# Kernel optimization log

Measured on AMD Instinct MI355X. Metric: run time of the kernel, lower is better.

The kernel has to match this reference:

```python
import jax, jax.numpy as jnp
import numpy as np

N_TOK = 4096      # total packed tokens
C = 256           # channels
H = 8             # num_heads
B = 8             # number of packed sequences
NEG = -10000.0    # additive mask value used by the torch module (not -inf)


def setup_inputs() -> dict:
    key = jax.random.key(0)
    ks = jax.random.split(key, 8)
    qkv = jax.random.normal(ks[0], (N_TOK, C), jnp.float32)
    q_pos = jax.random.normal(ks[1], (N_TOK, C), jnp.float32)
    # cu_seqlens: sorted prefix boundaries, 0 ... N_TOK (B segments)
    interior = jnp.sort(jax.random.randint(ks[2], (B - 1,), 1, N_TOK))
    cu_seqlens = jnp.concatenate([jnp.zeros((1,), jnp.int32),
                                  interior.astype(jnp.int32),
                                  jnp.full((1,), N_TOK, jnp.int32)])
    # xavier-uniform-ish scale for linear weights (stored as [in, out])
    def xavier(k, fan_in, fan_out):
        lim = np.sqrt(6.0 / (fan_in + fan_out)).astype(np.float32)
        return jax.random.uniform(k, (fan_in, fan_out), jnp.float32, -lim, lim)
    Wq = xavier(ks[3], C, C)
    Wkv = xavier(ks[4], C, 2 * C)
    Wproj = xavier(ks[5], C, C)
    bproj = jnp.zeros((C,), jnp.float32)
    return {"qkv": qkv, "q_pos": q_pos, "cu_seqlens": cu_seqlens,
            "max_seqlen": N_TOK, "Wq": Wq, "Wkv": Wkv,
            "Wproj": Wproj, "bproj": bproj}


def reference(qkv, q_pos, cu_seqlens, max_seqlen, Wq, Wkv, Wproj, bproj):
    N, Cdim = qkv.shape
    hd = Cdim // H
    scale = hd ** -0.5

    q = (qkv + q_pos) @ Wq                 # [N, C]
    kv = qkv @ Wkv                         # [N, 2C]
    k, v = kv[:, :Cdim], kv[:, Cdim:]

    # upcast_attention=True -> float32 attention (inputs already fp32)
    q = q.astype(jnp.float32).reshape(N, H, hd)
    k = k.astype(jnp.float32).reshape(N, H, hd)
    v = v.astype(jnp.float32).reshape(N, H, hd)

    # block-diagonal additive mask: segment id per token via searchsorted
    seg = jnp.searchsorted(cu_seqlens[1:], jnp.arange(N), side='right')
    bias = jnp.where(seg[:, None] == seg[None, :], 0.0, NEG)  # [N, N]

    scores = jnp.einsum('nhd,mhd->hnm', q, k) * scale + bias[None]  # [H,N,N]
    attn = jax.nn.softmax(scores, axis=-1)
    feat = jnp.einsum('hnm,mhd->nhd', attn, v).reshape(N, Cdim)
    feat = feat.astype(qkv.dtype)
    return feat @ Wproj + bproj
```

## Files before the change

### kernel.cpp

```cpp
#include <hip/hip_runtime.h>
#include <hip/hip_bf16.h>
#include <math.h>

#define NTOK 4096
#define CDIM 256
#define NH   8
#define HD   32
#define SCALE 0.17677669529663687f

typedef __attribute__((ext_vector_type(8))) short bf16x8;
typedef __attribute__((ext_vector_type(4))) short short4v;
typedef __attribute__((ext_vector_type(4))) float f32x4;

__device__ inline short f2b(float f) {
  union { __hip_bfloat16 h; short s; } u;
  u.h = __float2bfloat16(f);
  return u.s;
}
__device__ inline short4v pack4(f32x4 v) {
  short4v o; o[0] = f2b(v[0]); o[1] = f2b(v[1]); o[2] = f2b(v[2]); o[3] = f2b(v[3]);
  return o;
}

__global__ __launch_bounds__(256) void prep_kernel(
    const float* __restrict__ qkv, const float* __restrict__ qpos,
    const float* __restrict__ Wq, const float* __restrict__ Wkv,
    const float* __restrict__ Wp,
    short* __restrict__ Xq, short* __restrict__ X,
    short* __restrict__ WT, short* __restrict__ WpT)
{
  const int b = blockIdx.x, t = threadIdx.x;
  if (b < 1024) {
    const int i4 = (b * 256 + t) * 4;
    float4 a = *(const float4*)(qkv + i4);
    float4 p = *(const float4*)(qpos + i4);
    short4v xo, qo;
    xo[0] = f2b(a.x); xo[1] = f2b(a.y); xo[2] = f2b(a.z); xo[3] = f2b(a.w);
    qo[0] = f2b(a.x + p.x); qo[1] = f2b(a.y + p.y); qo[2] = f2b(a.z + p.z); qo[3] = f2b(a.w + p.w);
    *(short4v*)(X + i4)  = xo;
    *(short4v*)(Xq + i4) = qo;
  } else {
    const int gid = (b - 1024) * 256 + t;
    const int c  = gid & 1023;
    const int k4 = (gid >> 10) * 4;
    short4v o;
    if (c < 768) {
      #pragma unroll
      for (int j = 0; j < 4; ++j) {
        int k = k4 + j;
        float v = (c < 256) ? Wq[(size_t)k * 256 + c] * SCALE
                            : Wkv[(size_t)k * 512 + (c - 256)];
        o[j] = f2b(v);
      }
      *(short4v*)(WT + (size_t)c * 256 + k4) = o;
    } else {
      const int cc = c - 768;
      #pragma unroll
      for (int j = 0; j < 4; ++j) o[j] = f2b(Wp[(size_t)(k4 + j) * 256 + cc]);
      *(short4v*)(WpT + (size_t)cc * 256 + k4) = o;
    }
  }
}

__global__ __launch_bounds__(256) void gemm_qkv(
    const short* __restrict__ Xq, const short* __restrict__ X,
    const short* __restrict__ WT,
    short* __restrict__ qb, short* __restrict__ khp, short* __restrict__ vblk)
{
  __shared__ short Al[64][40];
  __shared__ short Wl[64][40];
  const int bx = blockIdx.x;
  const int n0 = blockIdx.y * 64;
  const int c0 = bx * 64;
  const int tid = threadIdx.x;
  const int w = tid >> 6, l = tid & 63, lg = l >> 4, lr = l & 15;
  const int wc = w & 1, wn = w >> 1;
  const short* A = (bx < 4) ? Xq : X;

  f32x4 acc[2][2];
  #pragma unroll
  for (int i = 0; i < 2; ++i)
    #pragma unroll
    for (int j = 0; j < 2; ++j) acc[i][j] = (f32x4){0.f, 0.f, 0.f, 0.f};

  for (int kt = 0; kt < 256; kt += 32) {
    __syncthreads();
    {
      int row = tid >> 2, seg = tid & 3;
      *(bf16x8*)&Al[row][seg * 8] = *(const bf16x8*)(A  + (size_t)(n0 + row) * 256 + kt + seg * 8);
      *(bf16x8*)&Wl[row][seg * 8] = *(const bf16x8*)(WT + (size_t)(c0 + row) * 256 + kt + seg * 8);
    }
    __syncthreads();
    bf16x8 wf[2], xf[2];
    #pragma unroll
    for (int ci = 0; ci < 2; ++ci) wf[ci] = *(bf16x8*)&Wl[wc * 32 + ci * 16 + lr][lg * 8];
    #pragma unroll
    for (int ni = 0; ni < 2; ++ni) xf[ni] = *(bf16x8*)&Al[wn * 32 + ni * 16 + lr][lg * 8];
    if (bx < 8) {
      #pragma unroll
      for (int ci = 0; ci < 2; ++ci)
        #pragma unroll
        for (int ni = 0; ni < 2; ++ni)
          acc[ci][ni] = __builtin_amdgcn_mfma_f32_16x16x32_bf16(wf[ci], xf[ni], acc[ci][ni], 0, 0, 0);
    } else {
      #pragma unroll
      for (int ci = 0; ci < 2; ++ci)
        #pragma unroll
        for (int ni = 0; ni < 2; ++ni)
          acc[ci][ni] = __builtin_amdgcn_mfma_f32_16x16x32_bf16(xf[ni], wf[ci], acc[ci][ni], 0, 0, 0);
    }
  }

  if (bx < 4) {
    const int cl0 = bx * 64;
    #pragma unroll
    for (int ci = 0; ci < 2; ++ci)
      #pragma unroll
      for (int ni = 0; ni < 2; ++ni) {
        int c = cl0 + wc * 32 + ci * 16 + lg * 4;
        int n = n0 + wn * 32 + ni * 16 + lr;
        *(short4v*)(qb + (size_t)n * 256 + c) = pack4(acc[ci][ni]);
      }
  } else if (bx < 8) {
    const int cl0 = (bx - 4) * 64;
    #pragma unroll
    for (int ci = 0; ci < 2; ++ci)
      #pragma unroll
      for (int ni = 0; ni < 2; ++ni) {
        int c = cl0 + wc * 32 + ci * 16 + lg * 4;
        int n = n0 + wn * 32 + ni * 16 + lr;
        int hh = c >> 5, d = c & 31;
        int tt = n >> 5, k = n & 31;
        int s = ((k >> 2) & 1) * 16 + (k >> 3) * 4 + (k & 3);
        *(short4v*)(khp + (((size_t)hh * 128 + tt) * 32 + s) * 32 + d) = pack4(acc[ci][ni]);
      }
  } else {
    const int cv0 = (bx - 8) * 64;
    #pragma unroll
    for (int ci = 0; ci < 2; ++ci)
      #pragma unroll
      for (int ni = 0; ni < 2; ++ni) {
        int c = cv0 + wc * 32 + ci * 16 + lr;
        int n = n0 + wn * 32 + ni * 16 + lg * 4;
        int hh = c >> 5, d = c & 31;
        int tt = n >> 5, k = n & 31;
        *(short4v*)(vblk + (((size_t)hh * 128 + tt) * 32 + d) * 32 + k) = pack4(acc[ci][ni]);
      }
  }
}

__global__ __launch_bounds__(256) void attn7(
    const short* __restrict__ qb, const short* __restrict__ khp,
    const short* __restrict__ vblk, const int* __restrict__ cu,
    short* __restrict__ featb)
{
  __shared__ float red[4][64][18];
  const int tid = threadIdx.x;
  const int w = tid >> 6, l = tid & 63, lg = l >> 4, lr = l & 15;
  const int bid = blockIdx.x;
  const int lid = ((bid & 7) << 7) | (bid >> 3);
  const int h = lid & 7, t32 = lid >> 3;
  const int n0 = t32 * 32;

  int cs[9];
  #pragma unroll
  for (int i = 0; i < 9; ++i) cs[i] = cu[i];

  const int qn0 = n0 + lr, qn1 = n0 + 16 + lr;
  int g0 = 0, g1 = 0, sg0 = 0, sgL = 0;
  #pragma unroll
  for (int j = 1; j <= 8; ++j) {
    g0  += (cs[j] <= qn0);
    g1  += (cs[j] <= qn1);
    sg0 += (cs[j] <= n0);
    sgL += (cs[j] <= n0 + 31);
  }
  const int kbeg0 = cs[g0], kend0 = cs[g0 + 1];
  const int kbeg1 = cs[g1], kend1 = cs[g1 + 1];
  const bool oneSeg = (sg0 == sgL);
  const int kbB = cs[sg0], keB = cs[sgL + 1];
  const int lo = kbB & ~31;
  const int hi = keB;
  const int t0 = lo >> 5;
  const int nT = (hi - lo + 31) >> 5;
  const int qT = (nT + 3) >> 2;
  const int it0 = w * qT;
  const int it1 = (it0 + qT < nT) ? (it0 + qT) : nT;

  const bf16x8 qf0 = *(const bf16x8*)(qb + (size_t)qn0 * 256 + h * 32 + lg * 8);
  const bf16x8 qf1 = *(const bf16x8*)(qb + (size_t)qn1 * 256 + h * 32 + lg * 8);
  const short* kL = khp  + (size_t)h * 131072 + lr * 32 + lg * 8;
  const short* vL = vblk + (size_t)h * 131072 + lr * 32 + lg * 8;

  f32x4 acc00 = {0.f,0.f,0.f,0.f}, acc01 = {0.f,0.f,0.f,0.f};
  f32x4 acc10 = {0.f,0.f,0.f,0.f}, acc11 = {0.f,0.f,0.f,0.f};
  float Lp0 = 0.f, Lp1 = 0.f;
  const f32x4 z4 = {0.f, 0.f, 0.f, 0.f};

  if (it0 < it1) {
    const short* kp = kL + (size_t)(t0 + it0) * 1024;
    const short* vp = vL + (size_t)(t0 + it0) * 1024;
    bf16x8 ka = *(const bf16x8*)(kp);
    bf16x8 kc = *(const bf16x8*)(kp + 512);
    bf16x8 va = *(const bf16x8*)(vp);
    bf16x8 vb = *(const bf16x8*)(vp + 512);
    for (int it = it0; it < it1; ++it) {
      const int itn = (it + 1 < it1) ? (it + 1) : it;
      const short* kpn = kL + (size_t)(t0 + itn) * 1024;
      const short* vpn = vL + (size_t)(t0 + itn) * 1024;
      bf16x8 kna = *(const bf16x8*)(kpn);
      bf16x8 knc = *(const bf16x8*)(kpn + 512);
      bf16x8 vna = *(const bf16x8*)(vpn);
      bf16x8 vnb = *(const bf16x8*)(vpn + 512);

      f32x4 s00 = __builtin_amdgcn_mfma_f32_16x16x32_bf16(ka, qf0, z4, 0, 0, 0);
      f32x4 s01 = __builtin_amdgcn_mfma_f32_16x16x32_bf16(kc, qf0, z4, 0, 0, 0);
      f32x4 s10 = __builtin_amdgcn_mfma_f32_16x16x32_bf16(ka, qf1, z4, 0, 0, 0);
      f32x4 s11 = __builtin_amdgcn_mfma_f32_16x16x32_bf16(kc, qf1, z4, 0, 0, 0);

      const int kt0 = (t0 + it) * 32;
      bf16x8 pf0, pf1;
      if (oneSeg & (kt0 >= kbB) & (kt0 + 32 <= keB)) {
        #pragma unroll
        for (int r = 0; r < 4; ++r) {
          float p00 = __expf(s00[r]), p01 = __expf(s01[r]);
          float p10 = __expf(s10[r]), p11 = __expf(s11[r]);
          Lp0 += p00 + p01; Lp1 += p10 + p11;
          pf0[r] = f2b(p00); pf0[4 + r] = f2b(p01);
          pf1[r] = f2b(p10); pf1[4 + r] = f2b(p11);
        }
      } else {
        const int kgb = kt0 + lg * 8;
        #pragma unroll
        for (int r = 0; r < 4; ++r) {
          int k0 = kgb + r, k1 = kgb + 4 + r;
          bool a00 = (k0 >= kbeg0) & (k0 < kend0);
          bool a01 = (k1 >= kbeg0) & (k1 < kend0);
          bool a10 = (k0 >= kbeg1) & (k0 < kend1);
          bool a11 = (k1 >= kbeg1) & (k1 < kend1);
          float p00 = a00 ? __expf(s00[r]) : 0.f;
          float p01 = a01 ? __expf(s01[r]) : 0.f;
          float p10 = a10 ? __expf(s10[r]) : 0.f;
          float p11 = a11 ? __expf(s11[r]) : 0.f;
          Lp0 += p00 + p01; Lp1 += p10 + p11;
          pf0[r] = f2b(p00); pf0[4 + r] = f2b(p01);
          pf1[r] = f2b(p10); pf1[4 + r] = f2b(p11);
        }
      }
      acc00 = __builtin_amdgcn_mfma_f32_16x16x32_bf16(pf0, va, acc00, 0, 0, 0);
      acc01 = __builtin_amdgcn_mfma_f32_16x16x32_bf16(pf0, vb, acc01, 0, 0, 0);
      acc10 = __builtin_amdgcn_mfma_f32_16x16x32_bf16(pf1, va, acc10, 0, 0, 0);
      acc11 = __builtin_amdgcn_mfma_f32_16x16x32_bf16(pf1, vb, acc11, 0, 0, 0);

      ka = kna; kc = knc; va = vna; vb = vnb;
    }
  }

  #pragma unroll
  for (int r = 0; r < 4; ++r) {
    red[w][l][r]      = acc00[r];
    red[w][l][4 + r]  = acc01[r];
    red[w][l][8 + r]  = acc10[r];
    red[w][l][12 + r] = acc11[r];
  }
  red[w][l][16] = Lp0;
  red[w][l][17] = Lp1;
  __syncthreads();
  if (w == 0) {
    float a00[4] = {0,0,0,0}, a01[4] = {0,0,0,0};
    float a10[4] = {0,0,0,0}, a11[4] = {0,0,0,0};
    float Ls0 = 0.f, Ls1 = 0.f;
    #pragma unroll
    for (int wv = 0; wv < 4; ++wv) {
      #pragma unroll
      for (int r = 0; r < 4; ++r) {
        a00[r] += red[wv][l][r];      a01[r] += red[wv][l][4 + r];
        a10[r] += red[wv][l][8 + r];  a11[r] += red[wv][l][12 + r];
      }
      Ls0 += red[wv][l][16];
      Ls1 += red[wv][l][17];
    }
    Ls0 += __shfl_xor(Ls0, 16); Ls0 += __shfl_xor(Ls0, 32);
    Ls1 += __shfl_xor(Ls1, 16); Ls1 += __shfl_xor(Ls1, 32);
    float inv0 = 1.f / Ls0, inv1 = 1.f / Ls1;
    #pragma unroll
    for (int r = 0; r < 4; ++r) {
      float i0 = __shfl(inv0, lg * 4 + r);
      float i1 = __shfl(inv1, lg * 4 + r);
      int na = n0 + lg * 4 + r;
      int nb = n0 + 16 + lg * 4 + r;
      featb[(size_t)na * 256 + h * 32 + lr]      = f2b(a00[r] * i0);
      featb[(size_t)na * 256 + h * 32 + 16 + lr] = f2b(a01[r] * i0);
      featb[(size_t)nb * 256 + h * 32 + lr]      = f2b(a10[r] * i1);
      featb[(size_t)nb * 256 + h * 32 + 16 + lr] = f2b(a11[r] * i1);
    }
  }
}

__global__ __launch_bounds__(256) void gemm_out(
    const short* __restrict__ Fb, const short* __restrict__ WpT,
    const float* __restrict__ bias, float* __restrict__ out)
{
  __shared__ short Al[64][40];
  __shared__ short Wl[64][40];
  const int c0 = blockIdx.x * 64;
  const int n0 = blockIdx.y * 64;
  const int tid = threadIdx.x;
  const int w = tid >> 6, l = tid & 63, lg = l >> 4, lr = l & 15;
  const int wc = w & 1, wn = w >> 1;

  f32x4 acc[2][2];
  #pragma unroll
  for (int i = 0; i < 2; ++i)
    #pragma unroll
    for (int j = 0; j < 2; ++j) acc[i][j] = (f32x4){0.f, 0.f, 0.f, 0.f};

  for (int kt = 0; kt < 256; kt += 32) {
    __syncthreads();
    {
      int row = tid >> 2, seg = tid & 3;
      *(bf16x8*)&Al[row][seg * 8] = *(const bf16x8*)(Fb  + (size_t)(n0 + row) * 256 + kt + seg * 8);
      *(bf16x8*)&Wl[row][seg * 8] = *(const bf16x8*)(WpT + (size_t)(c0 + row) * 256 + kt + seg * 8);
    }
    __syncthreads();
    bf16x8 wf[2], xf[2];
    #pragma unroll
    for (int ci = 0; ci < 2; ++ci) wf[ci] = *(bf16x8*)&Wl[wc * 32 + ci * 16 + lr][lg * 8];
    #pragma unroll
    for (int ni = 0; ni < 2; ++ni) xf[ni] = *(bf16x8*)&Al[wn * 32 + ni * 16 + lr][lg * 8];
    #pragma unroll
    for (int ci = 0; ci < 2; ++ci)
      #pragma unroll
      for (int ni = 0; ni < 2; ++ni)
        acc[ci][ni] = __builtin_amdgcn_mfma_f32_16x16x32_bf16(wf[ci], xf[ni], acc[ci][ni], 0, 0, 0);
  }

  #pragma unroll
  for (int ci = 0; ci < 2; ++ci)
    #pragma unroll
    for (int ni = 0; ni < 2; ++ni) {
      int c = c0 + wc * 32 + ci * 16 + lg * 4;
      int n = n0 + wn * 32 + ni * 16 + lr;
      f32x4 bv = *(const f32x4*)(bias + c);
      f32x4 o = acc[ci][ni] + bv;
      *(f32x4*)(out + (size_t)n * 256 + c) = o;
    }
}

extern "C" void kernel_launch(void* const* d_in, const int* in_sizes, int n_in,
                              void* d_out, int out_size, void* d_ws, size_t ws_size,
                              hipStream_t stream) {
  (void)in_sizes; (void)n_in; (void)out_size; (void)ws_size;
  const float* qkv   = (const float*)d_in[0];
  const float* q_pos = (const float*)d_in[1];
  const int*   cu    = (const int*)d_in[2];
  const float* Wq    = (const float*)d_in[4];
  const float* Wkv   = (const float*)d_in[5];
  const float* Wproj = (const float*)d_in[6];
  const float* bproj = (const float*)d_in[7];
  float* out = (float*)d_out;

  const size_t M = (size_t)NTOK * CDIM;
  short* S    = (short*)d_ws;
  short* Xq   = S;
  short* X    = S + M;
  short* qb   = S + 2 * M;
  short* khp  = S + 3 * M;
  short* vblk = S + 4 * M;
  short* Fb   = S + 5 * M;
  short* WT   = S + 6 * M;
  short* WpT  = WT + 768 * 256;

  prep_kernel<<<1280, 256, 0, stream>>>(qkv, q_pos, Wq, Wkv, Wproj, Xq, X, WT, WpT);
  gemm_qkv<<<dim3(12, 64), 256, 0, stream>>>(Xq, X, WT, qb, khp, vblk);
  attn7<<<1024, 256, 0, stream>>>(qb, khp, vblk, cu, Fb);
  gemm_out<<<dim3(4, 64), 256, 0, stream>>>(Fb, WpT, bproj, out);
}
```

Before: 39.48 us.

## Fold log2e into Q scale, use exp2, compute softmax denominator via MFMA

Folds log2(e) into the Q weight scaling so the softmax can use exp2f instead of __expf. The row sums are no longer accumulated on the VALU with cross-lane shuffles; two extra MFMAs against a vector of bf16 ones now produce them. The block-to-(head,tile) mapping changes from head-interleaved to head-major. The sums now come from the bf16-rounded probabilities, which keeps numerator and denominator consistent, at the cost of two extra MFMAs per iteration.

```diff
diff --git a/kernel.cpp b/kernel.cpp
--- a/kernel.cpp
+++ b/kernel.cpp
@@ -6,7 +6,7 @@
 #define CDIM 256
 #define NH   8
 #define HD   32
-#define SCALE 0.17677669529663687f
+#define QSCALE 0.2550565445517151f
 
 typedef __attribute__((ext_vector_type(8))) short bf16x8;
 typedef __attribute__((ext_vector_type(4))) short short4v;
@@ -48,7 +48,7 @@
       #pragma unroll
       for (int j = 0; j < 4; ++j) {
         int k = k4 + j;
-        float v = (c < 256) ? Wq[(size_t)k * 256 + c] * SCALE
+        float v = (c < 256) ? Wq[(size_t)k * 256 + c] * QSCALE
                             : Wkv[(size_t)k * 512 + (c - 256)];
         o[j] = f2b(v);
       }
@@ -149,17 +149,16 @@
   }
 }
 
-__global__ __launch_bounds__(256) void attn7(
+__global__ __launch_bounds__(256) void attn11(
     const short* __restrict__ qb, const short* __restrict__ khp,
     const short* __restrict__ vblk, const int* __restrict__ cu,
     short* __restrict__ featb)
 {
-  __shared__ float red[4][64][18];
+  __shared__ float red[4][64][24];
   const int tid = threadIdx.x;
   const int w = tid >> 6, l = tid & 63, lg = l >> 4, lr = l & 15;
   const int bid = blockIdx.x;
-  const int lid = ((bid & 7) << 7) | (bid >> 3);
-  const int h = lid & 7, t32 = lid >> 3;
+  const int h = bid >> 7, t32 = bid & 127;
   const int n0 = t32 * 32;
 
   int cs[9];
@@ -194,8 +193,11 @@
 
   f32x4 acc00 = {0.f,0.f,0.f,0.f}, acc01 = {0.f,0.f,0.f,0.f};
   f32x4 acc10 = {0.f,0.f,0.f,0.f}, acc11 = {0.f,0.f,0.f,0.f};
-  float Lp0 = 0.f, Lp1 = 0.f;
+  f32x4 accL0 = {0.f,0.f,0.f,0.f}, accL1 = {0.f,0.f,0.f,0.f};
   const f32x4 z4 = {0.f, 0.f, 0.f, 0.f};
+  bf16x8 ones;
+  #pragma unroll
+  for (int j = 0; j < 8; ++j) ones[j] = (short)0x3F80;
 
   if (it0 < it1) {
     const short* kp = kL + (size_t)(t0 + it0) * 1024;
@@ -223,11 +225,10 @@
       if (oneSeg & (kt0 >= kbB) & (kt0 + 32 <= keB)) {
         #pragma unroll
         for (int r = 0; r < 4; ++r) {
-          float p00 = __expf(s00[r]), p01 = __expf(s01[r]);
-          float p10 = __expf(s10[r]), p11 = __expf(s11[r]);
-          Lp0 += p00 + p01; Lp1 += p10 + p11;
-          pf0[r] = f2b(p00); pf0[4 + r] = f2b(p01);
-          pf1[r] = f2b(p10); pf1[4 + r] = f2b(p11);
+          pf0[r]     = f2b(exp2f(s00[r]));
+          pf0[4 + r] = f2b(exp2f(s01[r]));
+          pf1[r]     = f2b(exp2f(s10[r]));
+          pf1[4 + r] = f2b(exp2f(s11[r]));
         }
       } else {
         const int kgb = kt0 + lg * 8;
@@ -238,19 +239,18 @@
           bool a01 = (k1 >= kbeg0) & (k1 < kend0);
           bool a10 = (k0 >= kbeg1) & (k0 < kend1);
           bool a11 = (k1 >= kbeg1) & (k1 < kend1);
-          float p00 = a00 ? __expf(s00[r]) : 0.f;
-          float p01 = a01 ? __expf(s01[r]) : 0.f;
-          float p10 = a10 ? __expf(s10[r]) : 0.f;
-          float p11 = a11 ? __expf(s11[r]) : 0.f;
-          Lp0 += p00 + p01; Lp1 += p10 + p11;
-          pf0[r] = f2b(p00); pf0[4 + r] = f2b(p01);
-          pf1[r] = f2b(p10); pf1[4 + r] = f2b(p11);
+          pf0[r]     = f2b(a00 ? exp2f(s00[r]) : 0.f);
+          pf0[4 + r] = f2b(a01 ? exp2f(s01[r]) : 0.f);
+          pf1[r]     = f2b(a10 ? exp2f(s10[r]) : 0.f);
+          pf1[4 + r] = f2b(a11 ? exp2f(s11[r]) : 0.f);
         }
       }
       acc00 = __builtin_amdgcn_mfma_f32_16x16x32_bf16(pf0, va, acc00, 0, 0, 0);
       acc01 = __builtin_amdgcn_mfma_f32_16x16x32_bf16(pf0, vb, acc01, 0, 0, 0);
       acc10 = __builtin_amdgcn_mfma_f32_16x16x32_bf16(pf1, va, acc10, 0, 0, 0);
       acc11 = __builtin_amdgcn_mfma_f32_16x16x32_bf16(pf1, vb, acc11, 0, 0, 0);
+      accL0 = __builtin_amdgcn_mfma_f32_16x16x32_bf16(pf0, ones, accL0, 0, 0, 0);
+      accL1 = __builtin_amdgcn_mfma_f32_16x16x32_bf16(pf1, ones, accL1, 0, 0, 0);
 
       ka = kna; kc = knc; va = vna; vb = vnb;
     }
@@ -262,31 +262,27 @@
     red[w][l][4 + r]  = acc01[r];
     red[w][l][8 + r]  = acc10[r];
     red[w][l][12 + r] = acc11[r];
-  }
-  red[w][l][16] = Lp0;
-  red[w][l][17] = Lp1;
+    red[w][l][16 + r] = accL0[r];
+    red[w][l][20 + r] = accL1[r];
+  }
   __syncthreads();
   if (w == 0) {
     float a00[4] = {0,0,0,0}, a01[4] = {0,0,0,0};
     float a10[4] = {0,0,0,0}, a11[4] = {0,0,0,0};
-    float Ls0 = 0.f, Ls1 = 0.f;
+    float aL0[4] = {0,0,0,0}, aL1[4] = {0,0,0,0};
     #pragma unroll
     for (int wv = 0; wv < 4; ++wv) {
       #pragma unroll
       for (int r = 0; r < 4; ++r) {
         a00[r] += red[wv][l][r];      a01[r] += red[wv][l][4 + r];
         a10[r] += red[wv][l][8 + r];  a11[r] += red[wv][l][12 + r];
-      }
-      Ls0 += red[wv][l][16];
-      Ls1 += red[wv][l][17];
-    }
-    Ls0 += __shfl_xor(Ls0, 16); Ls0 += __shfl_xor(Ls0, 32);
-    Ls1 += __shfl_xor(Ls1, 16); Ls1 += __shfl_xor(Ls1, 32);
-    float inv0 = 1.f / Ls0, inv1 = 1.f / Ls1;
+        aL0[r] += red[wv][l][16 + r]; aL1[r] += red[wv][l][20 + r];
+      }
+    }
     #pragma unroll
     for (int r = 0; r < 4; ++r) {
-      float i0 = __shfl(inv0, lg * 4 + r);
-      float i1 = __shfl(inv1, lg * 4 + r);
+      float i0 = 1.f / aL0[r];
+      float i1 = 1.f / aL1[r];
       int na = n0 + lg * 4 + r;
       int nb = n0 + 16 + lg * 4 + r;
       featb[(size_t)na * 256 + h * 32 + lr]      = f2b(a00[r] * i0);
@@ -373,6 +369,6 @@
 
   prep_kernel<<<1280, 256, 0, stream>>>(qkv, q_pos, Wq, Wkv, Wproj, Xq, X, WT, WpT);
   gemm_qkv<<<dim3(12, 64), 256, 0, stream>>>(Xq, X, WT, qb, khp, vblk);
-  attn7<<<1024, 256, 0, stream>>>(qb, khp, vblk, cu, Fb);
+  attn11<<<1024, 256, 0, stream>>>(qb, khp, vblk, cu, Fb);
   gemm_out<<<dim3(4, 64), 256, 0, stream>>>(Fb, WpT, bproj, out);
 }
```

New measurement: 54.22 us. 37.4% more time.
